# Kernel optimization log

Measured on AMD Instinct MI355X. Metric: run time of the kernel, lower is better.

The kernel has to match this reference:

```python
import jax, jax.numpy as jnp
import numpy as np

N = 16384      # instances (cells) per bag
IN = 2000      # input_dim (genes)
E1, E2 = 1024, 512   # encoder_dims
HID = 512      # hidden_dim
NH, HD = 8, 64 # num_heads, head_dim
LK = 256       # linformer_k
EPROJ_N = 10000  # fixed in-dim of E/F projections
NEXP, MH = 4, 256  # moe experts, moe hidden (= classifier_dims[0])
C1, C2, NC = 256, 128, 2


def _ln(x, g, b):
    m = jnp.mean(x, axis=-1, keepdims=True)
    v = jnp.var(x, axis=-1, keepdims=True)
    return (x - m) * jax.lax.rsqrt(v + 1e-5) * g + b


def setup_inputs() -> dict:
    key = jax.random.key(0)
    ks = jax.random.split(key, 24)
    s = 0.02
    f32 = jnp.float32
    inp = {
        'x': jax.random.normal(ks[0], (N, IN), dtype=f32),
        'enc_w1': jax.random.normal(ks[1], (IN, E1), dtype=f32) * s,
        'enc_b1': jnp.zeros((E1,), f32),
        'enc_w2': jax.random.normal(ks[2], (E1, E2), dtype=f32) * s,
        'enc_b2': jnp.zeros((E2,), f32),
        'enc_w3': jax.random.normal(ks[3], (E2, HID), dtype=f32) * s,
        'enc_b3': jnp.zeros((HID,), f32),
        'q_w': jax.random.normal(ks[4], (HID, HID), dtype=f32) * s,
        'q_b': jnp.zeros((HID,), f32),
        'k_w': jax.random.normal(ks[5], (HID, HID), dtype=f32) * s,
        'k_b': jnp.zeros((HID,), f32),
        'v_w': jax.random.normal(ks[6], (HID, HID), dtype=f32) * s,
        'v_b': jnp.zeros((HID,), f32),
        'o_w': jax.random.normal(ks[7], (HID, HID), dtype=f32) * s,
        'o_b': jnp.zeros((HID,), f32),
        'E_w': jax.random.normal(ks[8], (LK, EPROJ_N), dtype=f32) * s,  # nn.Linear(10000, k).weight
        'F_w': jax.random.normal(ks[9], (LK, EPROJ_N), dtype=f32) * s,
        'ln1_g': jnp.ones((HID,), f32), 'ln1_b': jnp.zeros((HID,), f32),
        'ln2_g': jnp.ones((HID,), f32), 'ln2_b': jnp.zeros((HID,), f32),
        'gate_w': jax.random.normal(ks[10], (HID, NEXP), dtype=f32) * s,
        'gate_b': jnp.zeros((NEXP,), f32),
        'moe_w1': jax.random.normal(ks[11], (NEXP, HID, MH), dtype=f32) * s,
        'moe_b1': jnp.zeros((NEXP, MH), f32),
        'moe_w2': jax.random.normal(ks[12], (NEXP, MH), dtype=f32) * s,
        'moe_b2': jnp.zeros((NEXP,), f32),
        'cls_w1': jax.random.normal(ks[13], (HID, C1), dtype=f32) * s,
        'cls_b1': jnp.zeros((C1,), f32),
        'cls_w2': jax.random.normal(ks[14], (C1, C2), dtype=f32) * s,
        'cls_b2': jnp.zeros((C2,), f32),
        'cls_w3': jax.random.normal(ks[15], (C2, NC), dtype=f32) * s,
        'cls_b3': jnp.zeros((NC,), f32),
    }
    return inp


def reference(x, enc_w1, enc_b1, enc_w2, enc_b2, enc_w3, enc_b3,
              q_w, q_b, k_w, k_b, v_w, v_b, o_w, o_b, E_w, F_w,
              ln1_g, ln1_b, ln2_g, ln2_b,
              gate_w, gate_b, moe_w1, moe_b1, moe_w2, moe_b2,
              cls_w1, cls_b1, cls_w2, cls_b2, cls_w3, cls_b3):
    # --- instance encoder (chunking in torch is math-equivalent to one pass) ---
    h = jax.nn.relu(x @ enc_w1 + enc_b1)
    h = jax.nn.relu(h @ enc_w2 + enc_b2)
    feat = jax.nn.relu(h @ enc_w3 + enc_b3)          # [N, HID]
    # dropouts / InstanceDropout are identity at inference

    # --- linformer attention (single bag, batch of 1) ---
    Q = (feat @ q_w + q_b).reshape(N, NH, HD).transpose(1, 0, 2)  # [H, N, D]
    K = (feat @ k_w + k_b).reshape(N, NH, HD).transpose(1, 0, 2)
    V = (feat @ v_w + v_b).reshape(N, NH, HD).transpose(1, 0, 2)
    # N > linformer_k and the torch inner check (seq_len <= weight.size(0)=LK)
    # is false, so E/F are bilinearly resized from [10000, LK] to [LK, N], then
    # transposed to [N, LK] (matches F.interpolate align_corners=False).
    E_m = jax.image.resize(E_w.T, (LK, N), method='bilinear').T   # [N, LK]
    F_m = jax.image.resize(F_w.T, (LK, N), method='bilinear').T   # [N, LK]
    Kc = jnp.einsum('hnd,nk->hkd', K, E_m)           # [H, LK, D]
    Vc = jnp.einsum('hnd,nk->hkd', V, F_m)           # [H, LK, D]
    scores = jax.nn.softmax(jnp.einsum('hnd,hkd->hnk', Q, Kc) * (HD ** -0.5), axis=-1)
    ao = jnp.einsum('hnk,hkd->hnd', scores, Vc)      # [H, N, D]
    attn_out = ao.transpose(1, 0, 2).reshape(N, HID) @ o_w + o_b

    att = _ln(attn_out + feat, ln1_g, ln1_b)
    att = _ln(att, ln2_g, ln2_b)                     # [N, HID]

    # --- MoE MIL aggregation: gated mixture of per-expert attention pooling ---
    gates = jax.nn.softmax(jnp.mean(att, axis=0) @ gate_w + gate_b)       # [E]
    Hm = jnp.tanh(jnp.einsum('nd,edh->enh', att, moe_w1) + moe_b1[:, None, :])
    sc = jnp.einsum('enh,eh->en', Hm, moe_w2) + moe_b2[:, None]           # [E, N]
    a = jax.nn.softmax(sc, axis=1)                   # per-expert instance attention
    attn_weights = gates @ a                         # [N]
    bag = attn_weights @ att                         # [HID]

    # --- classifier ---
    c = jax.nn.relu(bag @ cls_w1 + cls_b1)
    c = jax.nn.relu(c @ cls_w2 + cls_b2)
    disease = c @ cls_w3 + cls_b3                    # [NC]
    # use_domain_adaptation=False -> no domain output
    return (bag, disease, attn_weights)
```

## Files before the change

kernel.cpp:

```cpp
#include <hip/hip_runtime.h>

#define DI __device__ __forceinline__

DI float bf2f(unsigned short u){ unsigned int v = ((unsigned int)u)<<16; float f; __builtin_memcpy(&f,&v,4); return f; }
DI unsigned short f2bf(float f){ unsigned int v; __builtin_memcpy(&v,&f,4); v = v + 0x7FFFu + ((v>>16)&1u); return (unsigned short)(v>>16); }

typedef __attribute__((ext_vector_type(8))) short bf16x8;
typedef __attribute__((ext_vector_type(4))) float f32x4;

#define GLD_LDS16(src, dst) __builtin_amdgcn_global_load_lds( \
    (const __attribute__((address_space(1))) void*)(src), \
    (__attribute__((address_space(3))) void*)(dst), 16, 0, 0)

DI void barrier_() { asm volatile("" ::: "memory"); __builtin_amdgcn_s_barrier(); asm volatile("" ::: "memory"); }

template<int ACT>
__global__ __launch_bounds__(256) void gemm2_k(
    const unsigned short* __restrict__ A, const unsigned short* __restrict__ Bt,
    const float* __restrict__ bias, unsigned short* __restrict__ C,
    int K, int lda, int ldb, int ldc)
{
  __shared__ unsigned short As[8192];
  __shared__ unsigned short Bs[8192];
  const int tid = threadIdx.x, lane = tid & 63, wid = tid >> 6;
  const int wm = wid >> 1, wn = wid & 1;
  const int nx = gridDim.x;
  const int bid = blockIdx.x + nx*blockIdx.y;
  const int cpx = (nx*gridDim.y) >> 3;
  const int wg = (bid & 7)*cpx + (bid >> 3);
  const long long mBase = (long long)(wg / nx) << 7;
  const long long nBase = (long long)(wg % nx) << 7;
  const int q = lane >> 4, r15 = lane & 15;

  f32x4 acc[4][4];
#pragma unroll
  for (int i=0;i<4;i++)
#pragma unroll
    for (int j=0;j<4;j++)
#pragma unroll
      for (int r=0;r<4;r++) acc[i][j][r] = 0.f;

  const int nkt = K >> 6;
  for (int kt=0; kt<nkt; ++kt) {
    const int k0 = kt << 6;
#pragma unroll
    for (int it=0; it<4; ++it) {
      const int dbase = (it<<8) + (wid<<6);
      const int d = dbase + lane;
      const int row = d >> 3, cc = d & 7, sc = cc ^ (row & 7);
      GLD_LDS16(A + (mBase + row)*(long long)lda + k0 + (sc<<3), As + (dbase<<3));
      GLD_LDS16(Bt + (nBase + row)*(long long)ldb + k0 + (sc<<3), Bs + (dbase<<3));
    }
    __syncthreads();
#pragma unroll
    for (int ks=0; ks<2; ++ks) {
      bf16x8 af[4], bfr[4];
#pragma unroll
      for (int mi=0; mi<4; ++mi) {
        const int row = (wm<<6) + (mi<<4) + r15;
        const int ch = ((ks<<2)+q) ^ (row&7);
        af[mi] = *(const bf16x8*)(As + (row<<6) + (ch<<3));
      }
#pragma unroll
      for (int ni=0; ni<4; ++ni) {
        const int col = (wn<<6) + (ni<<4) + r15;
        const int ch = ((ks<<2)+q) ^ (col&7);
        bfr[ni] = *(const bf16x8*)(Bs + (col<<6) + (ch<<3));
      }
#pragma unroll
      for (int mi=0; mi<4; ++mi)
#pragma unroll
        for (int ni=0; ni<4; ++ni)
          acc[mi][ni] = __builtin_amdgcn_mfma_f32_16x16x32_bf16(af[mi], bfr[ni], acc[mi][ni], 0, 0, 0);
    }
    __syncthreads();
  }
#pragma unroll
  for (int ni=0; ni<4; ++ni) {
    const long long n = nBase + (wn<<6) + (ni<<4) + r15;
    const float bval = bias[n];
#pragma unroll
    for (int mi=0; mi<4; ++mi) {
#pragma unroll
      for (int r=0; r<4; ++r) {
        const long long m = mBase + (wm<<6) + (mi<<4) + (q<<2) + r;
        float v = acc[mi][ni][r] + bval;
        if constexpr (ACT==1) v = fmaxf(v, 0.f);
        C[m*(long long)ldc + n] = f2bf(v);
      }
    }
  }
}

template<int ACT, bool MOE>
__global__ __launch_bounds__(512,2) void gemm4_k(
    const unsigned short* __restrict__ A, const unsigned short* __restrict__ Bt,
    const float* __restrict__ bias, unsigned short* __restrict__ C,
    const float* __restrict__ w2, float* __restrict__ scp,
    int K, int lda, int ldb, int ldc)
{
  __shared__ unsigned short As[2][16384];
  __shared__ unsigned short Bs[2][16384];
  const int tid = threadIdx.x, lane = tid & 63, wid = tid >> 6;
  const int wm = wid >> 2, wn = wid & 3;
  const int q = lane >> 4, r15 = lane & 15;
  const int nx = gridDim.x;
  const int bid = blockIdx.x + nx*blockIdx.y;
  const int cpx = (nx*gridDim.y) >> 3;
  const int wg = (bid & 7)*cpx + (bid >> 3);
  const long long mBase = (long long)(wg / nx) << 8;
  const long long nBase = (long long)(wg % nx) << 8;

  f32x4 acc[8][4];
#pragma unroll
  for (int i=0;i<8;i++)
#pragma unroll
    for (int j=0;j<4;j++)
#pragma unroll
      for (int r=0;r<4;r++) acc[i][j][r] = 0.f;

  const int NT = K >> 6;

#define G4_STA(j, nb, kk) { const int d_ = tid + ((j)<<9); const int row_ = d_>>3, c_ = d_&7, sc_ = c_ ^ (row_&7); \
    GLD_LDS16(A + (mBase+row_)*(long long)lda + (kk) + (sc_<<3), &As[nb][d_<<3]); }
#define G4_STB(j, nb, kk) { const int d_ = tid + ((j)<<9); const int row_ = d_>>3, c_ = d_&7, sc_ = c_ ^ (row_&7); \
    GLD_LDS16(Bt + (nBase+row_)*(long long)ldb + (kk) + (sc_<<3), &Bs[nb][d_<<3]); }

  G4_STB(0,0,0); G4_STB(1,0,0); G4_STB(2,0,0); G4_STB(3,0,0);
  G4_STA(0,0,0); G4_STA(2,0,0); G4_STA(1,0,0); G4_STA(3,0,0);

  for (int t=0; t<NT; ++t) {
    const int b = t & 1, nb = b ^ 1;
    const bool more = (t+1 < NT);
    const int k1 = (t+1) << 6;
    bf16x8 aF[8], bL[4], bH[4];

    asm volatile("s_waitcnt vmcnt(2)" ::: "memory");
    barrier_();
#pragma unroll
    for (int mi=0; mi<4; ++mi)
#pragma unroll
      for (int ks=0; ks<2; ++ks) {
        const int row = (wm<<7) + (mi<<4) + r15;
        const int ch = ((ks<<2)+q) ^ (row&7);
        aF[mi*2+ks] = *(const bf16x8*)&As[b][(row<<6) + (ch<<3)];
      }
#pragma unroll
    for (int ni=0; ni<2; ++ni)
#pragma unroll
      for (int ks=0; ks<2; ++ks) {
        const int col = (wn<<6) + (ni<<4) + r15;
        const int ch = ((ks<<2)+q) ^ (col&7);
        bL[ni*2+ks] = *(const bf16x8*)&Bs[b][(col<<6) + (ch<<3)];
      }
    if (more) { G4_STB(0,nb,k1); G4_STB(1,nb,k1); }
    __builtin_amdgcn_s_setprio(1);
#pragma unroll
    for (int mi=0; mi<4; ++mi)
#pragma unroll
      for (int ni=0; ni<2; ++ni)
#pragma unroll
        for (int ks=0; ks<2; ++ks)
          acc[mi][ni] = __builtin_amdgcn_mfma_f32_16x16x32_bf16(aF[mi*2+ks], bL[ni*2+ks], acc[mi][ni], 0,0,0);
    __builtin_amdgcn_s_setprio(0);
    barrier_();

#pragma unroll
    for (int ni=0; ni<2; ++ni)
#pragma unroll
      for (int ks=0; ks<2; ++ks) {
        const int col = (wn<<6) + ((ni+2)<<4) + r15;
        const int ch = ((ks<<2)+q) ^ (col&7);
        bH[ni*2+ks] = *(const bf16x8*)&Bs[b][(col<<6) + (ch<<3)];
      }
    if (more) { G4_STB(2,nb,k1); G4_STB(3,nb,k1); }
    __builtin_amdgcn_s_setprio(1);
#pragma unroll
    for (int mi=0; mi<4; ++mi)
#pragma unroll
      for (int ni=0; ni<2; ++ni)
#pragma unroll
        for (int ks=0; ks<2; ++ks)
          acc[mi][ni+2] = __builtin_amdgcn_mfma_f32_16x16x32_bf16(aF[mi*2+ks], bH[ni*2+ks], acc[mi][ni+2], 0,0,0);
    __builtin_amdgcn_s_setprio(0);

    if (more) { asm volatile("s_waitcnt vmcnt(4)" ::: "memory"); }
    else      { asm volatile("s_waitcnt vmcnt(0)" ::: "memory"); }
    barrier_();
#pragma unroll
    for (int mi=0; mi<4; ++mi)
#pragma unroll
      for (int ks=0; ks<2; ++ks) {
        const int row = (wm<<7) + ((mi+4)<<4) + r15;
        const int ch = ((ks<<2)+q) ^ (row&7);
        aF[mi*2+ks] = *(const bf16x8*)&As[b][(row<<6) + (ch<<3)];
      }
    if (more) { G4_STA(0,nb,k1); G4_STA(2,nb,k1); }
    __builtin_amdgcn_s_setprio(1);
#pragma unroll
    for (int mi=0; mi<4; ++mi)
#pragma unroll
      for (int ni=0; ni<2; ++ni)
#pragma unroll
        for (int ks=0; ks<2; ++ks)
          acc[mi+4][ni] = __builtin_amdgcn_mfma_f32_16x16x32_bf16(aF[mi*2+ks], bL[ni*2+ks], acc[mi+4][ni], 0,0,0);
    __builtin_amdgcn_s_setprio(0);
    barrier_();

    if (more) { G4_STA(1,nb,k1); G4_STA(3,nb,k1); }
    __builtin_amdgcn_s_setprio(1);
#pragma unroll
    for (int mi=0; mi<4; ++mi)
#pragma unroll
      for (int ni=0; ni<2; ++ni)
#pragma unroll
        for (int ks=0; ks<2; ++ks)
          acc[mi+4][ni+2] = __builtin_amdgcn_mfma_f32_16x16x32_bf16(aF[mi*2+ks], bH[ni*2+ks], acc[mi+4][ni+2], 0,0,0);
    __builtin_amdgcn_s_setprio(0);
  }
#undef G4_STA
#undef G4_STB

  if constexpr (MOE) {
    const int e = (int)(nBase >> 8);
#pragma unroll
    for (int mi=0; mi<8; ++mi) {
#pragma unroll
      for (int r=0; r<4; ++r) {
        float p = 0.f;
#pragma unroll
        for (int ni=0; ni<4; ++ni) {
          const int n = (int)nBase + (wn<<6) + (ni<<4) + r15;
          const float v = acc[mi][ni][r] + bias[n];
          const float th = 1.f - 2.f/(__expf(2.f*v) + 1.f);
          p += th * w2[n];
        }
        p += __shfl_xor(p,1,64); p += __shfl_xor(p,2,64);
        p += __shfl_xor(p,4,64); p += __shfl_xor(p,8,64);
        if (r15 == 0) {
          const long long m = mBase + (wm<<7) + (mi<<4) + (q<<2) + r;
          atomicAdd(scp + ((long long)e<<14) + m, p);
        }
      }
    }
  } else {
#pragma unroll
    for (int ni=0; ni<4; ++ni) {
      const long long n = nBase + (wn<<6) + (ni<<4) + r15;
      const float bval = bias[n];
#pragma unroll
      for (int mi=0; mi<8; ++mi) {
#pragma unroll
        for (int r=0; r<4; ++r) {
          const long long m = mBase + (wm<<7) + (mi<<4) + (q<<2) + r;
          float v = acc[mi][ni][r] + bval;
          if constexpr (ACT==1) v = fmaxf(v, 0.f);
          C[m*(long long)ldc + n] = f2bf(v);
        }
      }
    }
  }
}

DI void transpose64(const float* __restrict__ src, unsigned short* __restrict__ dst,
                    int K, int N, int Kpad, int k0, int n0, float (*tile)[65], int tid)
{
  const int c = tid & 63, rg = tid >> 6;
#pragma unroll
  for (int j=0;j<16;j++){
    const int r = (j<<2) + rg;
    const int k = k0 + r;
    tile[r][c] = (k < K) ? src[(long long)k*N + n0 + c] : 0.f;
  }
  __syncthreads();
#pragma unroll
  for (int j=0;j<16;j++){
    const int nn = (j<<2) + rg;
    dst[(long long)(n0+nn)*Kpad + k0 + c] = f2bf(tile[c][nn]);
  }
}

__global__ __launch_bounds__(256) void prep_k(
    const float* __restrict__ x, unsigned short* __restrict__ xb,
    const float* __restrict__ enc_w1, unsigned short* __restrict__ w1t,
    const float* __restrict__ enc_w2, unsigned short* __restrict__ w2t,
    const float* __restrict__ enc_w3, const float* __restrict__ q_w,
    const float* __restrict__ k_w, const float* __restrict__ v_w, const float* __restrict__ o_w,
    unsigned short* __restrict__ w3t, unsigned short* __restrict__ qkvw, unsigned short* __restrict__ owt,
    const float* __restrict__ moe_w1, unsigned short* __restrict__ mwt,
    const float* __restrict__ Ew, const float* __restrict__ Fw, float* __restrict__ t1,
    const float* __restrict__ qb, const float* __restrict__ kb, const float* __restrict__ vb,
    float* __restrict__ qkvb)
{
  __shared__ float tile[64][65];
  const int b = blockIdx.x, tid = threadIdx.x;
  if (b < 4096) {
#pragma unroll
    for (int i=0;i<4;i++){
      const long long cid = (long long)b*1024 + i*256 + tid;
      const long long row = cid >> 8; const int c = (int)(cid & 255);
      bf16x8 v;
      if (c < 250) {
        const float* p = x + row*2000 + c*8;
        const float4 f0 = *(const float4*)p, f1 = *(const float4*)(p+4);
        v[0]=(short)f2bf(f0.x); v[1]=(short)f2bf(f0.y); v[2]=(short)f2bf(f0.z); v[3]=(short)f2bf(f0.w);
        v[4]=(short)f2bf(f1.x); v[5]=(short)f2bf(f1.y); v[6]=(short)f2bf(f1.z); v[7]=(short)f2bf(f1.w);
      } else {
#pragma unroll
        for (int j=0;j<8;j++) v[j]=0;
      }
      *(bf16x8*)(xb + (cid<<3)) = v;
    }
  } else if (b < 4608) {
    const int bb = b - 4096;
    transpose64(enc_w1, w1t, 2000, 1024, 2048, (bb&31)<<6, (bb>>5)<<6, tile, tid);
  } else if (b < 4736) {
    const int bb = b - 4608;
    transpose64(enc_w2, w2t, 1024, 512, 1024, (bb&15)<<6, (bb>>4)<<6, tile, tid);
  } else if (b < 5056) {
    const int bb = b - 4736;
    const int z = bb >> 6, r = bb & 63;
    const float* s = (z==0)?enc_w3:(z==1)?q_w:(z==2)?k_w:(z==3)?v_w:o_w;
    unsigned short* d = (z==0)?w3t:(z==1)?qkvw:(z==2)?(qkvw+512*512):(z==3)?(qkvw+1024*512):owt;
    transpose64(s, d, 512, 512, 512, (r&7)<<6, (r>>3)<<6, tile, tid);
  } else if (b < 5184) {
    const int bb = b - 5056;
    const int z = bb >> 5, r = bb & 31;
    transpose64(moe_w1 + (long long)z*512*256, mwt + (long long)z*256*512,
                512, 256, 512, (r&7)<<6, (r>>3)<<6, tile, tid);
  } else {
    const int bb = b - 5184;
    const int k = bb & 255, which = bb >> 8, c = tid;
    if (which == 0 && k < 3) {
      const float* src = (k==0) ? qb : (k==1) ? kb : vb;
      qkvb[k*512 + c]       = src[c];
      qkvb[k*512 + 256 + c] = src[256 + c];
    }
    const float* W = which ? Fw : Ew;
    const float ksc = 39.0625f;
    const float inv = 1.f/39.0625f;
    const float sf = (k + 0.5f)*ksc - 0.5f;
    int ilo = (int)ceilf(sf - ksc); if (ilo < 0) ilo = 0;
    int ihi = (int)floorf(sf + ksc); if (ihi > 9999) ihi = 9999;
    float acc = 0.f, wsum = 0.f;
    for (int i=ilo; i<=ihi; ++i) {
      const float w = 1.f - fabsf(sf - (float)i)*inv;
      if (w > 0.f) { acc += w * W[c*10000 + i]; wsum += w; }
    }
    t1[(which*256 + k)*256 + c] = acc / wsum;
  }
}

__global__ __launch_bounds__(512) void red_k(const unsigned short* __restrict__ qkv,
                                             float* __restrict__ red)
{
  const int c = blockIdx.x, which = blockIdx.y, j = threadIdx.x;
  const unsigned short* X = qkv + (which ? 1024 : 512);
  int nlo = 64*c - 32; if (nlo < 0) nlo = 0;
  int nhi = 64*c + 95; if (nhi > 16383) nhi = 16383;
  float acc = 0.f;
  for (int n=nlo; n<=nhi; ++n) {
    float sf = (n + 0.5f)*0.015625f - 0.5f;
    sf = fminf(fmaxf(sf, 0.f), 255.f);
    const int c0 = (int)sf;
    const float f = sf - (float)c0;
    float w = 0.f;
    if (c == c0) w = 1.f - f;
    else if (c == c0+1) w = f;
    if (w != 0.f) acc += w * bf2f(X[(long long)n*1536 + j]);
  }
  red[(which*256 + c)*512 + j] = acc;
}

__global__ __launch_bounds__(512) void kc_k(const float* __restrict__ t1, const float* __restrict__ red,
                                            unsigned short* __restrict__ Kc, unsigned short* __restrict__ Vct)
{
  const int k = blockIdx.x, which = blockIdx.y, j = threadIdx.x;
  const float* T = t1 + (which*256 + k)*256;
  const float* R = red + which*131072;
  float acc = 0.f;
  for (int c=0; c<256; ++c) acc += T[c] * R[c*512 + j];
  const int h = j >> 6, d = j & 63;
  if (which == 0) Kc [(h<<14) + (k<<6) + d] = f2bf(acc);
  else            Vct[(h<<14) + (d<<8) + k] = f2bf(acc);
}

__global__ __launch_bounds__(256) void attn_k(
    const unsigned short* __restrict__ Qg, const unsigned short* __restrict__ Kc,
    const unsigned short* __restrict__ Vct, unsigned short* __restrict__ ao)
{
  __shared__ unsigned short Ks[16384];
  __shared__ unsigned short Vs[16384];
  __shared__ unsigned short Ps[32768];
  const int h = blockIdx.y;
  const long long mBase = (long long)blockIdx.x << 7;
  const int tid = threadIdx.x, lane = tid & 63, wid = tid >> 6;
  const int q = lane >> 4, r15 = lane & 15;

#pragma unroll
  for (int it=0; it<8; ++it) {
    const int dbase = (it<<8) + (wid<<6);
    const int d = dbase + lane;
    {
      const int row = d >> 3, cc = d & 7, sc = cc ^ (row & 7);
      GLD_LDS16(Kc + (h<<14) + (row<<6) + (sc<<3), Ks + (dbase<<3));
    }
    {
      const int row = d >> 5, cc = d & 31, sc = (cc & 24) | ((cc ^ (row & 7)) & 7);
      GLD_LDS16(Vct + (h<<14) + (row<<8) + (sc<<3), Vs + (dbase<<3));
    }
  }
  __syncthreads();

  f32x4 acc[2][16];
#pragma unroll
  for (int mi=0;mi<2;mi++)
#pragma unroll
    for (int ni=0;ni<16;ni++)
#pragma unroll
      for (int r=0;r<4;r++) acc[mi][ni][r] = 0.f;

#pragma unroll
  for (int ks=0; ks<2; ++ks) {
    bf16x8 af[2];
#pragma unroll
    for (int mi=0; mi<2; ++mi) {
      const long long m = mBase + (wid<<5) + (mi<<4) + r15;
      af[mi] = *(const bf16x8*)(Qg + m*1536 + (h<<6) + (ks<<5) + (q<<3));
    }
#pragma unroll
    for (int ni=0; ni<16; ++ni) {
      const int col = (ni<<4) + r15;
      const int ch = ((ks<<2)+q) ^ (col&7);
      const bf16x8 bv = *(const bf16x8*)(Ks + (col<<6) + (ch<<3));
      acc[0][ni] = __builtin_amdgcn_mfma_f32_16x16x32_bf16(af[0], bv, acc[0][ni], 0,0,0);
      acc[1][ni] = __builtin_amdgcn_mfma_f32_16x16x32_bf16(af[1], bv, acc[1][ni], 0,0,0);
    }
  }

#pragma unroll
  for (int mi=0; mi<2; ++mi) {
#pragma unroll
    for (int r=0; r<4; ++r) {
      float mx = -3.4e38f;
#pragma unroll
      for (int ni=0; ni<16; ++ni) mx = fmaxf(mx, acc[mi][ni][r]);
      mx = fmaxf(mx, __shfl_xor(mx,1,64)); mx = fmaxf(mx, __shfl_xor(mx,2,64));
      mx = fmaxf(mx, __shfl_xor(mx,4,64)); mx = fmaxf(mx, __shfl_xor(mx,8,64));
      float s = 0.f;
#pragma unroll
      for (int ni=0; ni<16; ++ni) {
        const float e = __expf((acc[mi][ni][r] - mx)*0.125f);
        acc[mi][ni][r] = e; s += e;
      }
      s += __shfl_xor(s,1,64); s += __shfl_xor(s,2,64);
      s += __shfl_xor(s,4,64); s += __shfl_xor(s,8,64);
      const float inv = 1.f / s;
      const int row = (wid<<5) + (mi<<4) + (q<<2) + r;
#pragma unroll
      for (int ni=0; ni<16; ++ni) {
        const int col = (ni<<4) + r15;
        const int ch = col >> 3;
        const int chs = (ch & 24) | ((ch ^ (row & 7)) & 7);
        Ps[(row<<8) + (chs<<3) + (col&7)] = f2bf(acc[mi][ni][r]*inv);
      }
    }
  }
  __syncthreads();

  f32x4 o[2][4];
#pragma unroll
  for (int mi=0;mi<2;mi++)
#pragma unroll
    for (int ni=0;ni<4;ni++)
#pragma unroll
      for (int r=0;r<4;r++) o[mi][ni][r] = 0.f;

#pragma unroll
  for (int kk=0; kk<8; ++kk) {
    bf16x8 pa[2];
#pragma unroll
    for (int mi=0; mi<2; ++mi) {
      const int row = (wid<<5) + (mi<<4) + r15;
      const int ch = (kk<<2) + q;
      const int chs = (ch & 24) | ((ch ^ (row & 7)) & 7);
      pa[mi] = *(const bf16x8*)(Ps + (row<<8) + (chs<<3));
    }
#pragma unroll
    for (int ni=0; ni<4; ++ni) {
      const int vrow = (ni<<4) + r15;
      const int ch = (kk<<2) + q;
      const int chs = (ch & 24) | ((ch ^ (vrow & 7)) & 7);
      const bf16x8 bv = *(const bf16x8*)(Vs + (vrow<<8) + (chs<<3));
      o[0][ni] = __builtin_amdgcn_mfma_f32_16x16x32_bf16(pa[0], bv, o[0][ni], 0,0,0);
      o[1][ni] = __builtin_amdgcn_mfma_f32_16x16x32_bf16(pa[1], bv, o[1][ni], 0,0,0);
    }
  }
#pragma unroll
  for (int mi=0; mi<2; ++mi)
#pragma unroll
    for (int ni=0; ni<4; ++ni)
#pragma unroll
      for (int r=0; r<4; ++r) {
        const long long m = mBase + (wid<<5) + (mi<<4) + (q<<2) + r;
        ao[m*512 + (h<<6) + (ni<<4) + r15] = f2bf(o[mi][ni][r]);
      }
}

__global__ __launch_bounds__(256) void ln64_k(
    const unsigned short* __restrict__ attno, const unsigned short* __restrict__ feat,
    const float* __restrict__ g1, const float* __restrict__ b1,
    const float* __restrict__ g2, const float* __restrict__ b2,
    unsigned short* __restrict__ att, float* __restrict__ colp, float* __restrict__ scp)
{
  __shared__ float cred[4][512];
  const int tid = threadIdx.x, lane = tid & 63, wid = tid >> 6;
  const int c0 = lane << 3;
  scp[((long long)blockIdx.x<<8) + tid] = 0.f;
  float g1v[8], b1v[8], g2v[8], b2v[8];
#pragma unroll
  for (int j=0;j<8;j++){ g1v[j]=g1[c0+j]; b1v[j]=b1[c0+j]; g2v[j]=g2[c0+j]; b2v[j]=b2[c0+j]; }
  float cacc[8];
#pragma unroll
  for (int j=0;j<8;j++) cacc[j]=0.f;
  for (int rr=0; rr<16; ++rr) {
    const long long row = ((long long)blockIdx.x<<6) + (rr<<2) + wid;
    const bf16x8 a = *(const bf16x8*)(attno + (row<<9) + c0);
    const bf16x8 f = *(const bf16x8*)(feat  + (row<<9) + c0);
    float xv[8]; float s=0.f, qs=0.f;
#pragma unroll
    for (int j=0;j<8;j++){ xv[j] = bf2f((unsigned short)a[j]) + bf2f((unsigned short)f[j]); s += xv[j]; qs += xv[j]*xv[j]; }
#pragma unroll
    for (int o=32;o;o>>=1){ s += __shfl_xor(s,o,64); qs += __shfl_xor(qs,o,64); }
    float m = s*(1.f/512.f);
    float rs = rsqrtf(qs*(1.f/512.f) - m*m + 1e-5f);
    float y[8]; s=0.f; qs=0.f;
#pragma unroll
    for (int j=0;j<8;j++){ y[j] = (xv[j]-m)*rs*g1v[j] + b1v[j]; s += y[j]; qs += y[j]*y[j]; }
#pragma unroll
    for (int o=32;o;o>>=1){ s += __shfl_xor(s,o,64); qs += __shfl_xor(qs,o,64); }
    m = s*(1.f/512.f);
    rs = rsqrtf(qs*(1.f/512.f) - m*m + 1e-5f);
    bf16x8 ov;
#pragma unroll
    for (int j=0;j<8;j++){ const float z = (y[j]-m)*rs*g2v[j] + b2v[j]; cacc[j] += z; ov[j] = (short)f2bf(z); }
    *(bf16x8*)(att + (row<<9) + c0) = ov;
  }
#pragma unroll
  for (int j=0;j<8;j++) cred[wid][c0+j] = cacc[j];
  __syncthreads();
  {
    const float v0 = cred[0][tid]+cred[1][tid]+cred[2][tid]+cred[3][tid];
    const float v1 = cred[0][tid+256]+cred[1][tid+256]+cred[2][tid+256]+cred[3][tid+256];
    colp[((long long)blockIdx.x<<9)+tid]     = v0;
    colp[((long long)blockIdx.x<<9)+tid+256] = v1;
  }
}

__global__ __launch_bounds__(512) void meangates_k(const float* __restrict__ part,
    const float* __restrict__ gw, const float* __restrict__ gb, float* __restrict__ gates)
{
  __shared__ float mv[512];
  __shared__ float tmp[4];
  const int t = threadIdx.x;
  float s = 0.f;
  for (int b=0;b<256;b++) s += part[(b<<9)+t];
  mv[t] = s * (1.f/16384.f);
  __syncthreads();
  if (t < 4) {
    float a = gb[t];
    for (int d=0; d<512; ++d) a += mv[d]*gw[d*4+t];
    tmp[t] = a;
  }
  __syncthreads();
  if (t == 0) {
    const float m = fmaxf(fmaxf(tmp[0],tmp[1]),fmaxf(tmp[2],tmp[3]));
    float e[4]; float ss=0.f;
    for (int i=0;i<4;i++){ e[i]=__expf(tmp[i]-m); ss+=e[i]; }
    for (int i=0;i<4;i++) gates[i] = e[i]/ss;
  }
}

__global__ __launch_bounds__(1024) void moestat_k(const float* __restrict__ sc,
                                                  float* __restrict__ mstat, float* __restrict__ sstat)
{
  __shared__ float red[1024];
  const int e = blockIdx.x, t = threadIdx.x;
  const float* p = sc + e*16384;
  float m = -3.4e38f;
  for (int n=t; n<16384; n+=1024) m = fmaxf(m, p[n]);
  red[t] = m; __syncthreads();
  for (int o=512;o;o>>=1){ if (t<o) red[t]=fmaxf(red[t],red[t+o]); __syncthreads(); }
  m = red[0]; __syncthreads();
  float s = 0.f;
  for (int n=t; n<16384; n+=1024) s += __expf(p[n]-m);
  red[t] = s; __syncthreads();
  for (int o=512;o;o>>=1){ if (t<o) red[t]+=red[t+o]; __syncthreads(); }
  if (t==0){ mstat[e]=m; sstat[e]=red[0]; }
}

__global__ __launch_bounds__(256) void wbag_k(const unsigned short* __restrict__ att,
    const float* __restrict__ scp, const float* __restrict__ gates,
    const float* __restrict__ mstat, const float* __restrict__ sstat,
    float* __restrict__ part, float* __restrict__ dout)
{
  __shared__ float wrow[128];
  const int c = threadIdx.x;
  const long long r0 = (long long)blockIdx.x * 128;
  if (c < 128) {
    const long long n = r0 + c;
    float w = 0.f;
#pragma unroll
    for (int e=0;e<4;e++) w += gates[e]*__expf(scp[((long long)e<<14)+n]-mstat[e]) / sstat[e];
    wrow[c] = w;
    dout[514 + n] = w;
  }
  __syncthreads();
  float a0=0.f, a1=0.f;
  for (int r=0;r<128;r++){
    const float w = wrow[r];
    const unsigned short* p = att + ((r0+r)<<9);
    a0 += w*bf2f(p[c]); a1 += w*bf2f(p[c+256]);
  }
  part[((long long)blockIdx.x<<9)+c]     = a0;
  part[((long long)blockIdx.x<<9)+c+256] = a1;
}

__global__ __launch_bounds__(512) void cls2_k(const float* __restrict__ bagp,
    const float* __restrict__ w1, const float* __restrict__ b1,
    const float* __restrict__ w2, const float* __restrict__ b2,
    const float* __restrict__ w3, const float* __restrict__ b3, float* __restrict__ dout)
{
  __shared__ float bag[512]; __shared__ float c1[256]; __shared__ float c2[128];
  const int tid = threadIdx.x;
  float s = 0.f;
  for (int b=0;b<128;b++) s += bagp[(b<<9)+tid];
  bag[tid] = s; dout[tid] = s;
  __syncthreads();
  if (tid < 256) {
    float a = b1[tid];
    for (int d=0; d<512; ++d) a += bag[d]*w1[d*256+tid];
    c1[tid] = fmaxf(a, 0.f);
  }
  __syncthreads();
  if (tid < 128) {
    float a2 = b2[tid];
    for (int d=0; d<256; ++d) a2 += c1[d]*w2[d*128+tid];
    c2[tid] = fmaxf(a2, 0.f);
  }
  __syncthreads();
  if (tid < 2) {
    float a3 = b3[tid];
    for (int d=0; d<128; ++d) a3 += c2[d]*w3[d*2+tid];
    dout[512 + tid] = a3;
  }
}

extern "C" void kernel_launch(void* const* d_in, const int* in_sizes, int n_in,
                              void* d_out, int out_size, void* d_ws, size_t ws_size,
                              hipStream_t stream)
{
  (void)in_sizes; (void)n_in; (void)out_size; (void)ws_size;
  const float* x      = (const float*)d_in[0];
  const float* enc_w1 = (const float*)d_in[1];
  const float* enc_b1 = (const float*)d_in[2];
  const float* enc_w2 = (const float*)d_in[3];
  const float* enc_b2 = (const float*)d_in[4];
  const float* enc_w3 = (const float*)d_in[5];
  const float* enc_b3 = (const float*)d_in[6];
  const float* q_w    = (const float*)d_in[7];
  const float* q_b    = (const float*)d_in[8];
  const float* k_w    = (const float*)d_in[9];
  const float* k_b    = (const float*)d_in[10];
  const float* v_w    = (const float*)d_in[11];
  const float* v_b    = (const float*)d_in[12];
  const float* o_w    = (const float*)d_in[13];
  const float* o_b    = (const float*)d_in[14];
  const float* E_w    = (const float*)d_in[15];
  const float* F_w    = (const float*)d_in[16];
  const float* ln1_g  = (const float*)d_in[17];
  const float* ln1_b  = (const float*)d_in[18];
  const float* ln2_g  = (const float*)d_in[19];
  const float* ln2_b  = (const float*)d_in[20];
  const float* gate_w = (const float*)d_in[21];
  const float* gate_b = (const float*)d_in[22];
  const float* moe_w1 = (const float*)d_in[23];
  const float* moe_b1 = (const float*)d_in[24];
  const float* moe_w2 = (const float*)d_in[25];
  const float* cls_w1 = (const float*)d_in[27];
  const float* cls_b1 = (const float*)d_in[28];
  const float* cls_w2 = (const float*)d_in[29];
  const float* cls_b2 = (const float*)d_in[30];
  const float* cls_w3 = (const float*)d_in[31];
  const float* cls_b3 = (const float*)d_in[32];

  char* ws = (char*)d_ws;
  const size_t MB = 1024*1024;
  unsigned short* x_bf  = (unsigned short*)(ws + 0);
  unsigned short* h1    = (unsigned short*)(ws + 64*MB);
  unsigned short* h2    = (unsigned short*)(ws + 0);
  unsigned short* feat  = (unsigned short*)(ws + 16*MB);
  unsigned short* qkv   = (unsigned short*)(ws + 32*MB);
  unsigned short* ao    = (unsigned short*)(ws + 80*MB);
  unsigned short* attno = (unsigned short*)(ws + 0);
  unsigned short* att   = (unsigned short*)(ws + 96*MB);
  unsigned short* w1t   = (unsigned short*)(ws + 112*MB);
  unsigned short* w2t   = (unsigned short*)(ws + 116*MB);
  unsigned short* w3t   = (unsigned short*)(ws + 117*MB);
  unsigned short* qkvw  = (unsigned short*)(ws + 117*MB + 512*1024);
  unsigned short* owt   = (unsigned short*)(ws + 119*MB);
  unsigned short* mwt   = (unsigned short*)(ws + 119*MB + 512*1024);
  float*  t1b   = (float*)(ws + 120*MB + 512*1024);
  float*  redb  = (float*)(ws + 121*MB);
  unsigned short* Kcbf  = (unsigned short*)(ws + 122*MB);
  unsigned short* Vctbf = (unsigned short*)(ws + 122*MB + 256*1024);
  float*  colp  = (float*)(ws + 122*MB + 512*1024);
  float*  bagp  = (float*)(ws + 123*MB);
  float*  qkvb  = (float*)(ws + 123*MB + 256*1024);
  float*  gatesp= (float*)(ws + 123*MB + 264*1024);
  float*  scp   = (float*)(ws + 123*MB + 268*1024);
  float*  mstat = (float*)(ws + 123*MB + 524*1024);
  float*  sstat = (float*)(ws + 123*MB + 524*1024 + 64);
  float*  dout  = (float*)d_out;

  prep_k<<<5696,256,0,stream>>>(x, x_bf, enc_w1, w1t, enc_w2, w2t,
                                enc_w3, q_w, k_w, v_w, o_w, w3t, qkvw, owt,
                                moe_w1, mwt, E_w, F_w, t1b, q_b, k_b, v_b, qkvb);

  gemm4_k<1,false><<<dim3(4,64,1),512,0,stream>>>(x_bf, w1t, enc_b1, h1, nullptr,nullptr, 2048,2048,2048,1024);
  gemm2_k<1><<<dim3(4,128,1),256,0,stream>>>(h1, w2t, enc_b2, h2,   1024,1024,1024, 512);
  gemm2_k<1><<<dim3(4,128,1),256,0,stream>>>(h2, w3t, enc_b3, feat,  512, 512, 512, 512);
  gemm4_k<0,false><<<dim3(6,64,1),512,0,stream>>>(feat, qkvw, qkvb, qkv, nullptr,nullptr, 512,512,512,1536);
  red_k<<<dim3(256,2),512,0,stream>>>(qkv, redb);
  kc_k <<<dim3(256,2),512,0,stream>>>(t1b, redb, Kcbf, Vctbf);
  attn_k<<<dim3(128,8),256,0,stream>>>(qkv, Kcbf, Vctbf, ao);
  gemm2_k<0><<<dim3(4,128,1),256,0,stream>>>(ao, owt, o_b, attno, 512,512,512,512);
  ln64_k<<<256,256,0,stream>>>(attno, feat, ln1_g, ln1_b, ln2_g, ln2_b, att, colp, scp);
  meangates_k<<<1,512,0,stream>>>(colp, gate_w, gate_b, gatesp);
  gemm4_k<0,true><<<dim3(4,64,1),512,0,stream>>>(att, mwt, moe_b1, nullptr, moe_w2, scp, 512,512,512,0);
  moestat_k<<<4,1024,0,stream>>>(scp, mstat, sstat);
  wbag_k<<<128,256,0,stream>>>(att, scp, gatesp, mstat, sstat, bagp, dout);
  cls2_k<<<1,512,0,stream>>>(bagp, cls_w1, cls_b1, cls_w2, cls_b2, cls_w3, cls_b3, dout);
}
```

Baseline: 473.8 us.

## Double-buffer 128x128 GEMM with quartered MFMA phases and reorder prep blocks

Replaces the single-buffered gemm2 kernel with gemm5, which double-buffers the LDS tiles. It prefetches the next K tile in four staggered slices interleaved with four MFMA quadrants, using explicit vmcnt waits, barriers and setprio. The QKV projection now also uses this kernel with a 12x128 grid instead of gemm4. The prep kernel moves the slow E/F interpolation blocks to the front and vectorises their loop, converts x four rows per block, and moves bias packing into its own block. The doubled LDS footprint and the launch_bounds min-blocks hint may limit occupancy or add register pressure.

```diff
diff --git a/kernel.cpp b/kernel.cpp
--- a/kernel.cpp
+++ b/kernel.cpp
@@ -15,22 +15,22 @@
 DI void barrier_() { asm volatile("" ::: "memory"); __builtin_amdgcn_s_barrier(); asm volatile("" ::: "memory"); }
 
 template<int ACT>
-__global__ __launch_bounds__(256) void gemm2_k(
+__global__ __launch_bounds__(256,2) void gemm5_k(
     const unsigned short* __restrict__ A, const unsigned short* __restrict__ Bt,
     const float* __restrict__ bias, unsigned short* __restrict__ C,
     int K, int lda, int ldb, int ldc)
 {
-  __shared__ unsigned short As[8192];
-  __shared__ unsigned short Bs[8192];
+  __shared__ unsigned short As[2][8192];
+  __shared__ unsigned short Bs[2][8192];
   const int tid = threadIdx.x, lane = tid & 63, wid = tid >> 6;
   const int wm = wid >> 1, wn = wid & 1;
+  const int q = lane >> 4, r15 = lane & 15;
   const int nx = gridDim.x;
   const int bid = blockIdx.x + nx*blockIdx.y;
   const int cpx = (nx*gridDim.y) >> 3;
   const int wg = (bid & 7)*cpx + (bid >> 3);
   const long long mBase = (long long)(wg / nx) << 7;
   const long long nBase = (long long)(wg % nx) << 7;
-  const int q = lane >> 4, r15 = lane & 15;
 
   f32x4 acc[4][4];
 #pragma unroll
@@ -40,41 +40,108 @@
 #pragma unroll
       for (int r=0;r<4;r++) acc[i][j][r] = 0.f;
 
-  const int nkt = K >> 6;
-  for (int kt=0; kt<nkt; ++kt) {
-    const int k0 = kt << 6;
-#pragma unroll
-    for (int it=0; it<4; ++it) {
-      const int dbase = (it<<8) + (wid<<6);
-      const int d = dbase + lane;
-      const int row = d >> 3, cc = d & 7, sc = cc ^ (row & 7);
-      GLD_LDS16(A + (mBase + row)*(long long)lda + k0 + (sc<<3), As + (dbase<<3));
-      GLD_LDS16(Bt + (nBase + row)*(long long)ldb + k0 + (sc<<3), Bs + (dbase<<3));
-    }
-    __syncthreads();
-#pragma unroll
-    for (int ks=0; ks<2; ++ks) {
-      bf16x8 af[4], bfr[4];
-#pragma unroll
-      for (int mi=0; mi<4; ++mi) {
+  const int NT = K >> 6;
+
+#define G5_STA(j, nb, kk) { const int d_ = tid + ((j)<<8); const int row_ = d_>>3, c_ = d_&7, sc_ = c_ ^ (row_&7); \
+    GLD_LDS16(A + (mBase+row_)*(long long)lda + (kk) + (sc_<<3), &As[nb][d_<<3]); }
+#define G5_STB(j, nb, kk) { const int d_ = tid + ((j)<<8); const int row_ = d_>>3, c_ = d_&7, sc_ = c_ ^ (row_&7); \
+    GLD_LDS16(Bt + (nBase+row_)*(long long)ldb + (kk) + (sc_<<3), &Bs[nb][d_<<3]); }
+
+  G5_STB(0,0,0); G5_STB(2,0,0); G5_STB(1,0,0); G5_STB(3,0,0);
+  G5_STA(0,0,0); G5_STA(2,0,0); G5_STA(1,0,0); G5_STA(3,0,0);
+
+  for (int t=0; t<NT; ++t) {
+    const int b = t & 1, nb = b ^ 1;
+    const bool more = (t+1 < NT);
+    const int k1 = (t+1) << 6;
+    bf16x8 aL[4], aH[4], bL[4], bH[4];
+
+    asm volatile("s_waitcnt vmcnt(2)" ::: "memory");
+    barrier_();
+#pragma unroll
+    for (int mi=0; mi<2; ++mi)
+#pragma unroll
+      for (int ks=0; ks<2; ++ks) {
         const int row = (wm<<6) + (mi<<4) + r15;
         const int ch = ((ks<<2)+q) ^ (row&7);
-        af[mi] = *(const bf16x8*)(As + (row<<6) + (ch<<3));
-      }
-#pragma unroll
-      for (int ni=0; ni<4; ++ni) {
+        aL[mi*2+ks] = *(const bf16x8*)&As[b][(row<<6) + (ch<<3)];
+      }
+#pragma unroll
+    for (int ni=0; ni<2; ++ni)
+#pragma unroll
+      for (int ks=0; ks<2; ++ks) {
         const int col = (wn<<6) + (ni<<4) + r15;
         const int ch = ((ks<<2)+q) ^ (col&7);
-        bfr[ni] = *(const bf16x8*)(Bs + (col<<6) + (ch<<3));
-      }
-#pragma unroll
-      for (int mi=0; mi<4; ++mi)
-#pragma unroll
-        for (int ni=0; ni<4; ++ni)
-          acc[mi][ni] = __builtin_amdgcn_mfma_f32_16x16x32_bf16(af[mi], bfr[ni], acc[mi][ni], 0, 0, 0);
-    }
-    __syncthreads();
-  }
+        bL[ni*2+ks] = *(const bf16x8*)&Bs[b][(col<<6) + (ch<<3)];
+      }
+    if (more) { G5_STB(0,nb,k1); G5_STB(2,nb,k1); }
+    __builtin_amdgcn_s_setprio(1);
+#pragma unroll
+    for (int mi=0; mi<2; ++mi)
+#pragma unroll
+      for (int ni=0; ni<2; ++ni)
+#pragma unroll
+        for (int ks=0; ks<2; ++ks)
+          acc[mi][ni] = __builtin_amdgcn_mfma_f32_16x16x32_bf16(aL[mi*2+ks], bL[ni*2+ks], acc[mi][ni], 0,0,0);
+    __builtin_amdgcn_s_setprio(0);
+    barrier_();
+
+#pragma unroll
+    for (int ni=0; ni<2; ++ni)
+#pragma unroll
+      for (int ks=0; ks<2; ++ks) {
+        const int col = (wn<<6) + ((ni+2)<<4) + r15;
+        const int ch = ((ks<<2)+q) ^ (col&7);
+        bH[ni*2+ks] = *(const bf16x8*)&Bs[b][(col<<6) + (ch<<3)];
+      }
+    if (more) { G5_STB(1,nb,k1); G5_STB(3,nb,k1); }
+    __builtin_amdgcn_s_setprio(1);
+#pragma unroll
+    for (int mi=0; mi<2; ++mi)
+#pragma unroll
+      for (int ni=0; ni<2; ++ni)
+#pragma unroll
+        for (int ks=0; ks<2; ++ks)
+          acc[mi][ni+2] = __builtin_amdgcn_mfma_f32_16x16x32_bf16(aL[mi*2+ks], bH[ni*2+ks], acc[mi][ni+2], 0,0,0);
+    __builtin_amdgcn_s_setprio(0);
+
+    if (more) { asm volatile("s_waitcnt vmcnt(4)" ::: "memory"); }
+    else      { asm volatile("s_waitcnt vmcnt(0)" ::: "memory"); }
+    barrier_();
+#pragma unroll
+    for (int mi=0; mi<2; ++mi)
+#pragma unroll
+      for (int ks=0; ks<2; ++ks) {
+        const int row = (wm<<6) + ((mi+2)<<4) + r15;
+        const int ch = ((ks<<2)+q) ^ (row&7);
+        aH[mi*2+ks] = *(const bf16x8*)&As[b][(row<<6) + (ch<<3)];
+      }
+    if (more) { G5_STA(0,nb,k1); G5_STA(2,nb,k1); }
+    __builtin_amdgcn_s_setprio(1);
+#pragma unroll
+    for (int mi=0; mi<2; ++mi)
+#pragma unroll
+      for (int ni=0; ni<2; ++ni)
+#pragma unroll
+        for (int ks=0; ks<2; ++ks)
+          acc[mi+2][ni] = __builtin_amdgcn_mfma_f32_16x16x32_bf16(aH[mi*2+ks], bL[ni*2+ks], acc[mi+2][ni], 0,0,0);
+    __builtin_amdgcn_s_setprio(0);
+    barrier_();
+
+    if (more) { G5_STA(1,nb,k1); G5_STA(3,nb,k1); }
+    __builtin_amdgcn_s_setprio(1);
+#pragma unroll
+    for (int mi=0; mi<2; ++mi)
+#pragma unroll
+      for (int ni=0; ni<2; ++ni)
+#pragma unroll
+        for (int ks=0; ks<2; ++ks)
+          acc[mi+2][ni+2] = __builtin_amdgcn_mfma_f32_16x16x32_bf16(aH[mi*2+ks], bH[ni*2+ks], acc[mi+2][ni+2], 0,0,0);
+    __builtin_amdgcn_s_setprio(0);
+  }
+#undef G5_STA
+#undef G5_STB
+
 #pragma unroll
   for (int ni=0; ni<4; ++ni) {
     const long long n = nBase + (wn<<6) + (ni<<4) + r15;
@@ -294,60 +361,78 @@
 {
   __shared__ float tile[64][65];
   const int b = blockIdx.x, tid = threadIdx.x;
-  if (b < 4096) {
-#pragma unroll
-    for (int i=0;i<4;i++){
-      const long long cid = (long long)b*1024 + i*256 + tid;
-      const long long row = cid >> 8; const int c = (int)(cid & 255);
-      bf16x8 v;
-      if (c < 250) {
-        const float* p = x + row*2000 + c*8;
-        const float4 f0 = *(const float4*)p, f1 = *(const float4*)(p+4);
-        v[0]=(short)f2bf(f0.x); v[1]=(short)f2bf(f0.y); v[2]=(short)f2bf(f0.z); v[3]=(short)f2bf(f0.w);
-        v[4]=(short)f2bf(f1.x); v[5]=(short)f2bf(f1.y); v[6]=(short)f2bf(f1.z); v[7]=(short)f2bf(f1.w);
-      } else {
-#pragma unroll
-        for (int j=0;j<8;j++) v[j]=0;
-      }
-      *(bf16x8*)(xb + (cid<<3)) = v;
-    }
-  } else if (b < 4608) {
-    const int bb = b - 4096;
+  if (b < 512) {
+    const int k = b & 255, which = b >> 8, c = tid;
+    const float* Wr = (which ? Fw : Ew) + (long long)c*10000;
+    const float ksc = 39.0625f, inv = 1.f/39.0625f;
+    const float sf = (k + 0.5f)*ksc - 0.5f;
+    int ilo = (int)ceilf(sf - ksc); if (ilo < 0) ilo = 0;
+    int ihi = (int)floorf(sf + ksc); if (ihi > 9999) ihi = 9999;
+    float acc = 0.f, wsum = 0.f;
+    int i = ilo;
+    for (; i + 8 <= ihi + 1; i += 8) {
+      float v[8], w[8];
+#pragma unroll
+      for (int j=0;j<8;j++) v[j] = Wr[i+j];
+#pragma unroll
+      for (int j=0;j<8;j++){
+        w[j] = fmaxf(1.f - fabsf(sf - (float)(i+j))*inv, 0.f);
+        acc += w[j]*v[j]; wsum += w[j];
+      }
+    }
+    for (; i <= ihi; ++i) {
+      const float w = fmaxf(1.f - fabsf(sf - (float)i)*inv, 0.f);
+      acc += w * Wr[i]; wsum += w;
+    }
+    t1[(which*256 + k)*256 + c] = acc / wsum;
+  } else if (b < 1024) {
+    const int bb = b - 512;
     transpose64(enc_w1, w1t, 2000, 1024, 2048, (bb&31)<<6, (bb>>5)<<6, tile, tid);
-  } else if (b < 4736) {
-    const int bb = b - 4608;
+  } else if (b < 1152) {
+    const int bb = b - 1024;
     transpose64(enc_w2, w2t, 1024, 512, 1024, (bb&15)<<6, (bb>>4)<<6, tile, tid);
-  } else if (b < 5056) {
-    const int bb = b - 4736;
+  } else if (b < 1472) {
+    const int bb = b - 1152;
     const int z = bb >> 6, r = bb & 63;
     const float* s = (z==0)?enc_w3:(z==1)?q_w:(z==2)?k_w:(z==3)?v_w:o_w;
     unsigned short* d = (z==0)?w3t:(z==1)?qkvw:(z==2)?(qkvw+512*512):(z==3)?(qkvw+1024*512):owt;
     transpose64(s, d, 512, 512, 512, (r&7)<<6, (r>>3)<<6, tile, tid);
-  } else if (b < 5184) {
-    const int bb = b - 5056;
+  } else if (b < 1600) {
+    const int bb = b - 1472;
     const int z = bb >> 5, r = bb & 31;
     transpose64(moe_w1 + (long long)z*512*256, mwt + (long long)z*256*512,
                 512, 256, 512, (r&7)<<6, (r>>3)<<6, tile, tid);
+  } else if (b == 1600) {
+#pragma unroll
+    for (int i=0;i<6;i++){
+      const int idx = i*256 + tid;
+      const int wq = idx >> 9, off = idx & 511;
+      const float* src = (wq==0)?qb:(wq==1)?kb:vb;
+      qkvb[idx] = src[off];
+    }
   } else {
-    const int bb = b - 5184;
-    const int k = bb & 255, which = bb >> 8, c = tid;
-    if (which == 0 && k < 3) {
-      const float* src = (k==0) ? qb : (k==1) ? kb : vb;
-      qkvb[k*512 + c]       = src[c];
-      qkvb[k*512 + 256 + c] = src[256 + c];
-    }
-    const float* W = which ? Fw : Ew;
-    const float ksc = 39.0625f;
-    const float inv = 1.f/39.0625f;
-    const float sf = (k + 0.5f)*ksc - 0.5f;
-    int ilo = (int)ceilf(sf - ksc); if (ilo < 0) ilo = 0;
-    int ihi = (int)floorf(sf + ksc); if (ihi > 9999) ihi = 9999;
-    float acc = 0.f, wsum = 0.f;
-    for (int i=ilo; i<=ihi; ++i) {
-      const float w = 1.f - fabsf(sf - (float)i)*inv;
-      if (w > 0.f) { acc += w * W[c*10000 + i]; wsum += w; }
-    }
-    t1[(which*256 + k)*256 + c] = acc / wsum;
+    const int bb = b - 1601;
+    const long long r0 = (long long)bb << 2;
+    const int c = tid;
+    if (c < 250) {
+      const float* p = x + r0*2000 + c*8;
+      float4 fa[4], fb[4];
+#pragma unroll
+      for (int rr=0; rr<4; ++rr){ fa[rr] = *(const float4*)(p + rr*2000); fb[rr] = *(const float4*)(p + rr*2000 + 4); }
+#pragma unroll
+      for (int rr=0; rr<4; ++rr){
+        bf16x8 v;
+        v[0]=(short)f2bf(fa[rr].x); v[1]=(short)f2bf(fa[rr].y); v[2]=(short)f2bf(fa[rr].z); v[3]=(short)f2bf(fa[rr].w);
+        v[4]=(short)f2bf(fb[rr].x); v[5]=(short)f2bf(fb[rr].y); v[6]=(short)f2bf(fb[rr].z); v[7]=(short)f2bf(fb[rr].w);
+        *(bf16x8*)(xb + (r0+rr)*2048 + (long long)c*8) = v;
+      }
+    } else {
+      bf16x8 z8;
+#pragma unroll
+      for (int j=0;j<8;j++) z8[j]=0;
+#pragma unroll
+      for (int rr=0; rr<4; ++rr) *(bf16x8*)(xb + (r0+rr)*2048 + (long long)c*8) = z8;
+    }
   }
 }
 
@@ -723,18 +808,18 @@
   float*  sstat = (float*)(ws + 123*MB + 524*1024 + 64);
   float*  dout  = (float*)d_out;
 
-  prep_k<<<5696,256,0,stream>>>(x, x_bf, enc_w1, w1t, enc_w2, w2t,
+  prep_k<<<5697,256,0,stream>>>(x, x_bf, enc_w1, w1t, enc_w2, w2t,
                                 enc_w3, q_w, k_w, v_w, o_w, w3t, qkvw, owt,
                                 moe_w1, mwt, E_w, F_w, t1b, q_b, k_b, v_b, qkvb);
 
   gemm4_k<1,false><<<dim3(4,64,1),512,0,stream>>>(x_bf, w1t, enc_b1, h1, nullptr,nullptr, 2048,2048,2048,1024);
-  gemm2_k<1><<<dim3(4,128,1),256,0,stream>>>(h1, w2t, enc_b2, h2,   1024,1024,1024, 512);
-  gemm2_k<1><<<dim3(4,128,1),256,0,stream>>>(h2, w3t, enc_b3, feat,  512, 512, 512, 512);
-  gemm4_k<0,false><<<dim3(6,64,1),512,0,stream>>>(feat, qkvw, qkvb, qkv, nullptr,nullptr, 512,512,512,1536);
+  gemm5_k<1><<<dim3(4,128,1),256,0,stream>>>(h1, w2t, enc_b2, h2,   1024,1024,1024, 512);
+  gemm5_k<1><<<dim3(4,128,1),256,0,stream>>>(h2, w3t, enc_b3, feat,  512, 512, 512, 512);
+  gemm5_k<0><<<dim3(12,128,1),256,0,stream>>>(feat, qkvw, qkvb, qkv, 512,512,512,1536);
   red_k<<<dim3(256,2),512,0,stream>>>(qkv, redb);
   kc_k <<<dim3(256,2),512,0,stream>>>(t1b, redb, Kcbf, Vctbf);
   attn_k<<<dim3(128,8),256,0,stream>>>(qkv, Kcbf, Vctbf, ao);
-  gemm2_k<0><<<dim3(4,128,1),256,0,stream>>>(ao, owt, o_b, attno, 512,512,512,512);
+  gemm5_k<0><<<dim3(4,128,1),256,0,stream>>>(ao, owt, o_b, attno, 512,512,512,512);
   ln64_k<<<256,256,0,stream>>>(attno, feat, ln1_g, ln1_b, ln2_g, ln2_b, att, colp, scp);
   meangates_k<<<1,512,0,stream>>>(colp, gate_w, gate_b, gatesp);
   gemm4_k<0,true><<<dim3(4,64,1),512,0,stream>>>(att, mwt, moe_b1, nullptr, moe_w2, scp, 512,512,512,0);
```

Result: faster. 431.8 us (-8.9%).
